# Kernel tuning notes

Hardware: AMD Instinct MI355X
Metric: run time of the kernel (lower is better)

## Reference

```python
import jax, jax.numpy as jnp
import numpy as np

ALPHA = 1.0


def setup_inputs() -> dict:
    key = jax.random.key(0)
    k1, k2 = jax.random.split(key)
    N, D, K = 262144, 256, 256
    x = jax.random.normal(k1, (N, D), dtype=jnp.float32)
    clusters = jax.random.normal(k2, (K, D), dtype=jnp.float32)
    return {"x": x, "clusters": clusters}


def reference(x, clusters):
    # Squared euclidean distance to each cluster center without materializing
    x_sq = jnp.sum(x * x, axis=1, keepdims=True)            # (N, 1)
    c_sq = jnp.sum(clusters * clusters, axis=1)[None, :]    # (1, K)
    cross = jnp.einsum('nd,kd->nk', x, clusters)            # (N, K)
    sq_dist = x_sq - 2.0 * cross + c_sq                     # (N, K)
    # Student-t kernel (as in t-SNE / DEC): q_ij = (1 + d^2/alpha)^(-(alpha+1)/2)
    q = 1.0 / (1.0 + sq_dist / ALPHA)
    q = q ** ((ALPHA + 1.0) / 2.0)
    # Row-normalize to soft assignment probabilities.
    q = q / jnp.sum(q, axis=1, keepdims=True)
    return q
```

## Files before the change

### kernel.cpp

```cpp
#include <hip/hip_runtime.h>


#define NROWS 262144
#define DDIM  256
#define KCL   256
#define TPB   16
#define GRID  (NROWS / 64 / TPB)

using f32x4  = __attribute__((ext_vector_type(4))) float;
using s16x8  = __attribute__((ext_vector_type(8))) short;

__device__ inline unsigned short f2bf(float f) {
    unsigned int u = __float_as_uint(f);
    u += 0x7fffu + ((u >> 16) & 1u);
    return (unsigned short)(u >> 16);
}

__global__ void prep_kernel(const float* __restrict__ clusters,
                            unsigned short* __restrict__ cb,
                            float* __restrict__ csq) {
    int k    = blockIdx.x;
    int lane = threadIdx.x;
    const float* row = clusters + (size_t)k * DDIM;
    float4 a = *reinterpret_cast<const float4*>(row + lane * 4);
    ushort4 b;
    b.x = f2bf(a.x); b.y = f2bf(a.y); b.z = f2bf(a.z); b.w = f2bf(a.w);
    *reinterpret_cast<ushort4*>(cb + (size_t)k * DDIM + lane * 4) = b;
    float ss = a.x*a.x + a.y*a.y + a.z*a.z + a.w*a.w;
    #pragma unroll
    for (int m = 1; m < 64; m <<= 1) ss += __shfl_xor(ss, m);
    if (lane == 0) csq[k] = ss;
}

__global__ __launch_bounds__(512, 2) void fused_kernel(
    const float* __restrict__ x,
    const unsigned short* __restrict__ cb,
    const float* __restrict__ csq,
    float* __restrict__ out) {

    __shared__ char  lds_b[KCL * DDIM * 2];
    __shared__ float ls_sum[TPB][2][4][16];
    __shared__ int   ls_flag[2][4];

    const int tid  = threadIdx.x;
    const int lane = tid & 63;
    const int wave = tid >> 6;
    const int rg   = wave >> 1;
    const int ch   = wave & 1;
    const int c15  = lane & 15;
    const int kch  = lane >> 4;

    const int tile0 = blockIdx.x * TPB;

    #pragma unroll
    for (int it = 0; it < 16; ++it) {
        int slot = it * 8192 + tid * 16;
        int src  = slot ^ (((slot >> 9) & 7) << 4);
        __builtin_amdgcn_global_load_lds(
            (const __attribute__((address_space(1))) unsigned int*)((const char*)cb + src),
            (__attribute__((address_space(3))) unsigned int*)(lds_b + slot),
            16, 0, 0);
    }

    if (tid < 8) ((int*)ls_flag)[tid] = 0;

    float cs[8];
    #pragma unroll
    for (int f = 0; f < 8; ++f) cs[f] = csq[ch * 128 + f * 16 + c15];

    __syncthreads();

    auto xrow = [&](int t) -> const float* {
        return x + (size_t)((tile0 + t) * 64 + rg * 16 + c15) * DDIM + kch * 8;
    };

    f32x4 xv1[8], xv2[8];

    {
        const float* xr = xrow(0);
        #pragma unroll
        for (int i = 0; i < 8; ++i)
            xv1[i] = *reinterpret_cast<const f32x4*>(xr + (i >> 1) * 32 + (i & 1) * 4);
    }

    #pragma unroll 1
    for (int t = 0; t < TPB; ++t) {
        const int trow = (tile0 + t) * 64;
        const float* xr = xrow(t);

        #pragma unroll
        for (int i = 0; i < 8; ++i) {
            int ii = 8 + i;
            xv2[i] = *reinterpret_cast<const f32x4*>(xr + (ii >> 1) * 32 + (ii & 1) * 4);
        }

        s16x8 afrag[8];
        float p[4] = {0.f, 0.f, 0.f, 0.f};

        #pragma unroll
        for (int s4 = 0; s4 < 4; ++s4) {
            f32x4 xa = xv1[2 * s4], xb = xv1[2 * s4 + 1];
            float t0 = xa[0]*xa[0] + xa[1]*xa[1];
            float t1 = xa[2]*xa[2] + xa[3]*xa[3];
            float t2 = xb[0]*xb[0] + xb[1]*xb[1];
            float t3 = xb[2]*xb[2] + xb[3]*xb[3];
            p[s4] += (t0 + t1) + (t2 + t3);
            afrag[s4][0] = (short)f2bf(xa[0]); afrag[s4][1] = (short)f2bf(xa[1]);
            afrag[s4][2] = (short)f2bf(xa[2]); afrag[s4][3] = (short)f2bf(xa[3]);
            afrag[s4][4] = (short)f2bf(xb[0]); afrag[s4][5] = (short)f2bf(xb[1]);
            afrag[s4][6] = (short)f2bf(xb[2]); afrag[s4][7] = (short)f2bf(xb[3]);
        }

        f32x4 acc[8];
        #pragma unroll
        for (int f = 0; f < 8; ++f) acc[f] = (f32x4){0.f, 0.f, 0.f, 0.f};

        __builtin_amdgcn_s_setprio(1);
        #pragma unroll
        for (int s = 0; s < 4; ++s) {
            #pragma unroll
            for (int f = 0; f < 8; ++f) {
                int ba = ((ch * 128 + f * 16 + c15) * 512) + s * 64 + kch * 16;
                ba ^= ((c15 & 7) << 4);
                s16x8 bfrag = *reinterpret_cast<const s16x8*>(lds_b + ba);
                acc[f] = __builtin_amdgcn_mfma_f32_16x16x32_bf16(afrag[s], bfrag,
                                                                 acc[f], 0, 0, 0);
            }
        }
        __builtin_amdgcn_s_setprio(0);

        #pragma unroll
        for (int s4 = 0; s4 < 4; ++s4) {
            f32x4 xa = xv2[2 * s4], xb = xv2[2 * s4 + 1];
            float t0 = xa[0]*xa[0] + xa[1]*xa[1];
            float t1 = xa[2]*xa[2] + xa[3]*xa[3];
            float t2 = xb[0]*xb[0] + xb[1]*xb[1];
            float t3 = xb[2]*xb[2] + xb[3]*xb[3];
            p[s4] += (t0 + t1) + (t2 + t3);
            int s = 4 + s4;
            afrag[s][0] = (short)f2bf(xa[0]); afrag[s][1] = (short)f2bf(xa[1]);
            afrag[s][2] = (short)f2bf(xa[2]); afrag[s][3] = (short)f2bf(xa[3]);
            afrag[s][4] = (short)f2bf(xb[0]); afrag[s][5] = (short)f2bf(xb[1]);
            afrag[s][6] = (short)f2bf(xb[2]); afrag[s][7] = (short)f2bf(xb[3]);
        }

        if (t + 1 < TPB) {
            const float* xn = xrow(t + 1);
            #pragma unroll
            for (int i = 0; i < 8; ++i)
                xv1[i] = *reinterpret_cast<const f32x4*>(xn + (i >> 1) * 32 + (i & 1) * 4);
        }

        __builtin_amdgcn_s_setprio(1);
        #pragma unroll
        for (int s = 4; s < 8; ++s) {
            #pragma unroll
            for (int f = 0; f < 8; ++f) {
                int ba = ((ch * 128 + f * 16 + c15) * 512) + s * 64 + kch * 16;
                ba ^= ((c15 & 7) << 4);
                s16x8 bfrag = *reinterpret_cast<const s16x8*>(lds_b + ba);
                acc[f] = __builtin_amdgcn_mfma_f32_16x16x32_bf16(afrag[s], bfrag,
                                                                 acc[f], 0, 0, 0);
            }
        }
        __builtin_amdgcn_s_setprio(0);

        float xsq = (p[0] + p[1]) + (p[2] + p[3]);
        xsq += __shfl_xor(xsq, 16);
        xsq += __shfl_xor(xsq, 32);

        float psum[4];
        #pragma unroll
        for (int r = 0; r < 4; ++r) {
            float xrr = __shfl(xsq, kch * 4 + r);
            float s = 0.f;
            #pragma unroll
            for (int f = 0; f < 8; ++f) {
                float d2 = xrr - 2.0f * acc[f][r] + cs[f];
                float qv = __builtin_amdgcn_rcpf(1.0f + d2);
                acc[f][r] = qv;
                s += qv;
            }
            s += __shfl_xor(s, 1);
            s += __shfl_xor(s, 2);
            s += __shfl_xor(s, 4);
            s += __shfl_xor(s, 8);
            psum[r] = s;
        }

        if (c15 == 0) {
            #pragma unroll
            for (int r = 0; r < 4; ++r)
                ls_sum[t][ch][rg][kch * 4 + r] = psum[r];
        }
        asm volatile("s_waitcnt lgkmcnt(0)" ::: "memory");
        if (lane == 0)
            __atomic_store_n(&ls_flag[ch][rg], t + 1, __ATOMIC_RELAXED);

        volatile int* pf = (volatile int*)&ls_flag[ch ^ 1][rg];
        while (*pf <= t) { __builtin_amdgcn_s_sleep(1); }
        asm volatile("" ::: "memory");

        const int row0t = trow + rg * 16;
        #pragma unroll
        for (int r = 0; r < 4; ++r) {
            float other = ls_sum[t][ch ^ 1][rg][kch * 4 + r];
            float inv = __builtin_amdgcn_rcpf(psum[r] + other);
            const size_t orow = (size_t)(row0t + kch * 4 + r) * KCL;
            #pragma unroll
            for (int f = 0; f < 8; ++f) {
                __builtin_nontemporal_store(acc[f][r] * inv,
                                            &out[orow + ch * 128 + f * 16 + c15]);
            }
        }
    }
}

extern "C" void kernel_launch(void* const* d_in, const int* in_sizes, int n_in,
                              void* d_out, int out_size, void* d_ws, size_t ws_size,
                              hipStream_t stream) {
    const float* x        = (const float*)d_in[0];
    const float* clusters = (const float*)d_in[1];
    float* out = (float*)d_out;

    unsigned short* cb  = (unsigned short*)d_ws;
    float*          csq = (float*)((char*)d_ws + (size_t)KCL * DDIM * sizeof(unsigned short));

    prep_kernel<<<KCL, 64, 0, stream>>>(clusters, cb, csq);
    fused_kernel<<<GRID, 512, 0, stream>>>(x, cb, csq, out);
}
```

Baseline: 126.6 us.

## Halve LDS cluster tile, stream other half of B from global/L2

The LDS copy of the bf16 cluster matrix is cut in half: each wave half keeps 64 cluster rows in LDS and reads the other 64 directly from global memory (L2-resident) per k-step. Tiles per block drop from 16 to 8, and the x registers are reduced to a single reused buffer, with loads for the second half issued after the first conversion. The bf16 conversion also switches to the library intrinsic. The aim is lower LDS footprint and register pressure, allowing more blocks per CU for better latency hiding, at the cost of extra global/L2 traffic for B fragments.

```diff
diff --git a/kernel.cpp b/kernel.cpp
--- a/kernel.cpp
+++ b/kernel.cpp
@@ -1,10 +1,11 @@
 #include <hip/hip_runtime.h>
+#include <hip/hip_bf16.h>
 
 
 #define NROWS 262144
 #define DDIM  256
 #define KCL   256
-#define TPB   16
+#define TPB   8
 #define GRID  (NROWS / 64 / TPB)
 
 using f32x4  = __attribute__((ext_vector_type(4))) float;
@@ -14,6 +15,10 @@
     unsigned int u = __float_as_uint(f);
     u += 0x7fffu + ((u >> 16) & 1u);
     return (unsigned short)(u >> 16);
+}
+
+__device__ inline short bfc(float f) {
+    return (short)__bfloat16_as_ushort(__float2bfloat16(f));
 }
 
 __global__ void prep_kernel(const float* __restrict__ clusters,
@@ -38,7 +43,7 @@
     const float* __restrict__ csq,
     float* __restrict__ out) {
 
-    __shared__ char  lds_b[KCL * DDIM * 2];
+    __shared__ char  lds_b[2 * 64 * DDIM * 2];
     __shared__ float ls_sum[TPB][2][4][16];
     __shared__ int   ls_flag[2][4];
 
@@ -53,12 +58,15 @@
     const int tile0 = blockIdx.x * TPB;
 
     #pragma unroll
-    for (int it = 0; it < 16; ++it) {
-        int slot = it * 8192 + tid * 16;
-        int src  = slot ^ (((slot >> 9) & 7) << 4);
+    for (int it = 0; it < 8; ++it) {
+        int lin    = it * 8192 + tid * 16;
+        int chunk  = lin >> 15;
+        int rowin  = (lin >> 9) & 63;
+        int inrow  = lin & 511;
+        int gsrc   = (chunk * 128 + rowin) * 512 + (inrow ^ ((rowin & 7) << 4));
         __builtin_amdgcn_global_load_lds(
-            (const __attribute__((address_space(1))) unsigned int*)((const char*)cb + src),
-            (__attribute__((address_space(3))) unsigned int*)(lds_b + slot),
+            (const __attribute__((address_space(1))) unsigned int*)((const char*)cb + gsrc),
+            (__attribute__((address_space(3))) unsigned int*)(lds_b + lin),
             16, 0, 0);
     }
 
@@ -67,6 +75,8 @@
     float cs[8];
     #pragma unroll
     for (int f = 0; f < 8; ++f) cs[f] = csq[ch * 128 + f * 16 + c15];
+
+    const unsigned short* gb = cb + (size_t)(ch * 128 + 64 + c15) * DDIM + kch * 8;
 
     __syncthreads();
 
@@ -74,41 +84,39 @@
         return x + (size_t)((tile0 + t) * 64 + rg * 16 + c15) * DDIM + kch * 8;
     };
 
-    f32x4 xv1[8], xv2[8];
-
-    {
-        const float* xr = xrow(0);
-        #pragma unroll
-        for (int i = 0; i < 8; ++i)
-            xv1[i] = *reinterpret_cast<const f32x4*>(xr + (i >> 1) * 32 + (i & 1) * 4);
-    }
+    f32x4 xv[8];
+
+    #pragma unroll
+    for (int i = 0; i < 8; ++i)
+        xv[i] = *reinterpret_cast<const f32x4*>(xrow(0) + (i >> 1) * 32 + (i & 1) * 4);
 
     #pragma unroll 1
     for (int t = 0; t < TPB; ++t) {
         const int trow = (tile0 + t) * 64;
         const float* xr = xrow(t);
 
-        #pragma unroll
-        for (int i = 0; i < 8; ++i) {
-            int ii = 8 + i;
-            xv2[i] = *reinterpret_cast<const f32x4*>(xr + (ii >> 1) * 32 + (ii & 1) * 4);
-        }
-
-        s16x8 afrag[8];
-        float p[4] = {0.f, 0.f, 0.f, 0.f};
-
+        float p0 = 0.f, p1 = 0.f;
+
+        s16x8 afA[4];
         #pragma unroll
         for (int s4 = 0; s4 < 4; ++s4) {
-            f32x4 xa = xv1[2 * s4], xb = xv1[2 * s4 + 1];
+            f32x4 xa = xv[2 * s4], xb = xv[2 * s4 + 1];
             float t0 = xa[0]*xa[0] + xa[1]*xa[1];
             float t1 = xa[2]*xa[2] + xa[3]*xa[3];
             float t2 = xb[0]*xb[0] + xb[1]*xb[1];
             float t3 = xb[2]*xb[2] + xb[3]*xb[3];
-            p[s4] += (t0 + t1) + (t2 + t3);
-            afrag[s4][0] = (short)f2bf(xa[0]); afrag[s4][1] = (short)f2bf(xa[1]);
-            afrag[s4][2] = (short)f2bf(xa[2]); afrag[s4][3] = (short)f2bf(xa[3]);
-            afrag[s4][4] = (short)f2bf(xb[0]); afrag[s4][5] = (short)f2bf(xb[1]);
-            afrag[s4][6] = (short)f2bf(xb[2]); afrag[s4][7] = (short)f2bf(xb[3]);
+            if (s4 & 1) p1 += (t0 + t1) + (t2 + t3);
+            else        p0 += (t0 + t1) + (t2 + t3);
+            afA[s4][0] = bfc(xa[0]); afA[s4][1] = bfc(xa[1]);
+            afA[s4][2] = bfc(xa[2]); afA[s4][3] = bfc(xa[3]);
+            afA[s4][4] = bfc(xb[0]); afA[s4][5] = bfc(xb[1]);
+            afA[s4][6] = bfc(xb[2]); afA[s4][7] = bfc(xb[3]);
+        }
+
+        #pragma unroll
+        for (int i = 0; i < 8; ++i) {
+            int ii = 8 + i;
+            xv[i] = *reinterpret_cast<const f32x4*>(xr + (ii >> 1) * 32 + (ii & 1) * 4);
         }
 
         f32x4 acc[8];
@@ -118,54 +126,71 @@
         __builtin_amdgcn_s_setprio(1);
         #pragma unroll
         for (int s = 0; s < 4; ++s) {
-            #pragma unroll
-            for (int f = 0; f < 8; ++f) {
-                int ba = ((ch * 128 + f * 16 + c15) * 512) + s * 64 + kch * 16;
+            s16x8 g[4];
+            #pragma unroll
+            for (int f4 = 0; f4 < 4; ++f4)
+                g[f4] = *reinterpret_cast<const s16x8*>(gb + (size_t)f4 * 16 * DDIM + s * 32);
+            #pragma unroll
+            for (int f4 = 0; f4 < 4; ++f4) {
+                int ba = ch * 32768 + ((f4 * 16 + c15) * 512) + s * 64 + kch * 16;
                 ba ^= ((c15 & 7) << 4);
                 s16x8 bfrag = *reinterpret_cast<const s16x8*>(lds_b + ba);
-                acc[f] = __builtin_amdgcn_mfma_f32_16x16x32_bf16(afrag[s], bfrag,
-                                                                 acc[f], 0, 0, 0);
-            }
+                acc[f4] = __builtin_amdgcn_mfma_f32_16x16x32_bf16(afA[s], bfrag,
+                                                                  acc[f4], 0, 0, 0);
+            }
+            #pragma unroll
+            for (int f4 = 0; f4 < 4; ++f4)
+                acc[4 + f4] = __builtin_amdgcn_mfma_f32_16x16x32_bf16(afA[s], g[f4],
+                                                                      acc[4 + f4], 0, 0, 0);
         }
         __builtin_amdgcn_s_setprio(0);
 
+        s16x8 afB[4];
         #pragma unroll
         for (int s4 = 0; s4 < 4; ++s4) {
-            f32x4 xa = xv2[2 * s4], xb = xv2[2 * s4 + 1];
+            f32x4 xa = xv[2 * s4], xb = xv[2 * s4 + 1];
             float t0 = xa[0]*xa[0] + xa[1]*xa[1];
             float t1 = xa[2]*xa[2] + xa[3]*xa[3];
             float t2 = xb[0]*xb[0] + xb[1]*xb[1];
             float t3 = xb[2]*xb[2] + xb[3]*xb[3];
-            p[s4] += (t0 + t1) + (t2 + t3);
-            int s = 4 + s4;
-            afrag[s][0] = (short)f2bf(xa[0]); afrag[s][1] = (short)f2bf(xa[1]);
-            afrag[s][2] = (short)f2bf(xa[2]); afrag[s][3] = (short)f2bf(xa[3]);
-            afrag[s][4] = (short)f2bf(xb[0]); afrag[s][5] = (short)f2bf(xb[1]);
-            afrag[s][6] = (short)f2bf(xb[2]); afrag[s][7] = (short)f2bf(xb[3]);
+            if (s4 & 1) p1 += (t0 + t1) + (t2 + t3);
+            else        p0 += (t0 + t1) + (t2 + t3);
+            afB[s4][0] = bfc(xa[0]); afB[s4][1] = bfc(xa[1]);
+            afB[s4][2] = bfc(xa[2]); afB[s4][3] = bfc(xa[3]);
+            afB[s4][4] = bfc(xb[0]); afB[s4][5] = bfc(xb[1]);
+            afB[s4][6] = bfc(xb[2]); afB[s4][7] = bfc(xb[3]);
         }
 
         if (t + 1 < TPB) {
             const float* xn = xrow(t + 1);
             #pragma unroll
             for (int i = 0; i < 8; ++i)
-                xv1[i] = *reinterpret_cast<const f32x4*>(xn + (i >> 1) * 32 + (i & 1) * 4);
+                xv[i] = *reinterpret_cast<const f32x4*>(xn + (i >> 1) * 32 + (i & 1) * 4);
         }
 
         __builtin_amdgcn_s_setprio(1);
         #pragma unroll
-        for (int s = 4; s < 8; ++s) {
-            #pragma unroll
-            for (int f = 0; f < 8; ++f) {
-                int ba = ((ch * 128 + f * 16 + c15) * 512) + s * 64 + kch * 16;
+        for (int s = 0; s < 4; ++s) {
+            s16x8 g[4];
+            #pragma unroll
+            for (int f4 = 0; f4 < 4; ++f4)
+                g[f4] = *reinterpret_cast<const s16x8*>(gb + (size_t)f4 * 16 * DDIM + (s + 4) * 32);
+            #pragma unroll
+            for (int f4 = 0; f4 < 4; ++f4) {
+                int ba = ch * 32768 + ((f4 * 16 + c15) * 512) + (s + 4) * 64 + kch * 16;
                 ba ^= ((c15 & 7) << 4);
                 s16x8 bfrag = *reinterpret_cast<const s16x8*>(lds_b + ba);
-                acc[f] = __builtin_amdgcn_mfma_f32_16x16x32_bf16(afrag[s], bfrag,
-                                                                 acc[f], 0, 0, 0);
-            }
+                acc[f4] = __builtin_amdgcn_mfma_f32_16x16x32_bf16(afB[s], bfrag,
+                                                                  acc[f4], 0, 0, 0);
+            }
+            #pragma unroll
+            for (int f4 = 0; f4 < 4; ++f4)
+                acc[4 + f4] = __builtin_amdgcn_mfma_f32_16x16x32_bf16(afB[s], g[f4],
+                                                                      acc[4 + f4], 0, 0, 0);
         }
         __builtin_amdgcn_s_setprio(0);
 
-        float xsq = (p[0] + p[1]) + (p[2] + p[3]);
+        float xsq = p0 + p1;
         xsq += __shfl_xor(xsq, 16);
         xsq += __shfl_xor(xsq, 32);
 
```

Result: slower. 216.8 us (+71.3%).
